# Performance work log

Measured on AMD Instinct MI355X. Metric: run time of the kernel, lower is better.

The kernel has to match this reference:

```python
import jax, jax.numpy as jnp
import numpy as np

# --- basis bookkeeping (mirrors TwoBodyToSpherical._generate_buffers) ---
METADATA = np.array([3, 2, 1], dtype=np.int64)          # shells per l
N_IRREPS = 2 * np.arange(3, dtype=np.int64) + 1          # 2l+1
REP_OFFSETS = np.concatenate([[0], np.cumsum(METADATA * N_IRREPS)[:-1]])
NUM_REPS_1D = int((METADATA * N_IRREPS).sum())           # = 14
M_IDX_MAP = {0: [0], 1: [0, 2, 1], 2: [0, 1, 2, 3, 4]}
ANGULAR = {"s": 0, "p": 1, "d": 2}

C_AOS = ["1s", "2s", "3s"] + ["2p"] * 3 + ["3p"] * 3 + ["3d"] * 5
H_AOS = ["1s", "2s"]


def _build_repid_map(aos):
    # faithful port of the per-element repid_map construction (valence_only=True)
    repid = np.zeros(len(aos), dtype=np.int64)
    dst_n, l_last, m_qc = 0, 0, 0
    for i, ao in enumerate(aos):
        l = ANGULAR[ao[1]]
        if l > l_last:
            dst_n = 0
        repid[i] = REP_OFFSETS[l] + dst_n + M_IDX_MAP[l][m_qc] * METADATA[l]
        if m_qc == 2 * l:
            m_qc = 0
            dst_n += 1
        else:
            m_qc += 1
        l_last = l
    return repid


def setup_inputs() -> dict:
    key = jax.random.key(0)
    maps = {"C": _build_repid_map(C_AOS), "H": _build_repid_map(H_AOS)}
    atomsybs = ["C"] * 400 + ["H"] * 100               # 500 atoms
    n_atoms = len(atomsybs)
    dst_rep_ids_1d = np.concatenate([maps[a] for a in atomsybs])
    lens = np.array([len(maps[a]) for a in atomsybs], dtype=np.int64)
    dst_offsets_1d = np.repeat(np.arange(n_atoms, dtype=np.int64), lens)
    dst_flat_ids_1d = dst_offsets_1d * NUM_REPS_1D + dst_rep_ids_1d  # [N_ao]=5800
    n_ao = dst_flat_ids_1d.shape[0]
    feat_ten = jax.random.normal(key, (n_ao, n_ao), dtype=jnp.float32)
    return {
        "feat_ten": feat_ten,
        "dst_flat_ids_1d": jnp.asarray(dst_flat_ids_1d, dtype=jnp.int32),
        "n_atoms": n_atoms,
        "num_reps_1d": NUM_REPS_1D,
    }


def reference(feat_ten, dst_flat_ids_1d, n_atoms, num_reps_1d):
    total = n_atoms * num_reps_1d                        # 7000
    # 2D destination flat ids: outer-sum of 1D ids (rep_dims=(0,1))
    ids2d = (dst_flat_ids_1d[:, None] * total + dst_flat_ids_1d[None, :]).reshape(-1)
    flat = feat_ten.reshape(-1)
    out_flat = jnp.zeros((total * total,), dtype=feat_ten.dtype).at[ids2d].add(flat)
    # view(n_atoms, R, n_atoms, R) then transpose(1,2) -> [A, A, R, R]
    out = out_flat.reshape(n_atoms, num_reps_1d, n_atoms, num_reps_1d)
    return jnp.transpose(out, (0, 2, 1, 3))
```

## Files before the change

kernel.cpp:

```cpp
#include <hip/hip_runtime.h>

constexpr int R = 14;
constexpr int A = 500;
constexpr int TOTAL = A * R;
constexpr int TILE = R * R;
constexpr int G = 25;
constexpr int NG = A / G;
constexpr int SUPER = 4;
constexpr int NSUP = NG / SUPER;
constexpr int MAXW = G * R;
constexpr int WP = 360;
constexpr int CHUNK = G * TILE;

__global__ __launch_bounds__(1024) void setup_kernel(
        const int* __restrict__ dst, int n_ao,
        int* __restrict__ inv, int* __restrict__ arow,
        int* __restrict__ ncols, int* __restrict__ pm) {
    int tid = threadIdx.x;
    for (int t = tid; t < TOTAL; t += 1024) inv[t] = -1;
    __syncthreads();
    for (int t = tid; t < n_ao; t += 1024) inv[dst[t]] = t;
    __syncthreads();
    if (tid < A) {
        int a = tid, lo = 0x7fffffff, hi = -1;
#pragma unroll
        for (int r = 0; r < R; ++r) {
            int v = inv[a * R + r];
            if (v >= 0) { lo = min(lo, v); hi = max(hi, v); }
        }
        arow[a] = lo;
        ncols[a] = hi - lo + 1;
#pragma unroll
        for (int r = 0; r < R; ++r) {
            int v = inv[a * R + r];
            pm[a * R + r] = (v >= 0) ? (v - lo) : -1;
        }
    }
}

__global__ __launch_bounds__(512) void tile_kernel(
        const float* __restrict__ feat,
        const int* __restrict__ arow,
        const int* __restrict__ ncols,
        const int* __restrict__ pm,
        float* __restrict__ out, int n_ao) {
    const int gs  = blockIdx.x % NSUP;
    const int a1  = blockIdx.x / NSUP;
    const int tid = threadIdx.x;

    __shared__ float buf[R][WP];
    __shared__ int s_pr[R];
    __shared__ int s_pc[G * R];
    __shared__ int s_off[G];

    const int arow1 = arow[a1];
    const int n1    = ncols[a1];
    if (tid < R) s_pr[tid] = pm[a1 * R + tid];

    const int d0 = tid >> 7;
    const int c4 = tid & 127;

    for (int s = 0; s < SUPER; ++s) {
        const int g0   = (gs * SUPER + s) * G;
        const int colL = arow[g0];
        const int colA = colL & ~3;
        const int colR = arow[g0 + G - 1] + ncols[g0 + G - 1];
        const int W4   = (colR - colA + 3) >> 2;

        for (int t = tid; t < G * R; t += 512) s_pc[t] = pm[g0 * R + t];
        if (tid < G) s_off[tid] = arow[g0 + tid] - colA;

        if (c4 < W4) {
            const float4* src4 =
                (const float4*)(feat + (long long)arow1 * n_ao + colA);
            const int rs4 = n_ao >> 2;
            for (int d = d0; d < n1; d += 4)
                *(float4*)&buf[d][c4 << 2] = src4[(long long)d * rs4 + c4];
        }
        __syncthreads();

        const long long outbase = ((long long)a1 * A + g0) * (long long)TILE;
        for (int o4 = tid * 4; o4 < CHUNK; o4 += 2048) {
            int a2i = o4 / TILE;
            int e   = o4 - a2i * TILE;
            int r1  = e / R;
            int r2  = e - r1 * R;
            int d   = s_pr[r1];
            int off = s_off[a2i];
            const int* pc = &s_pc[a2i * R];
            float4 v;
            float* vp = &v.x;
#pragma unroll
            for (int k = 0; k < 4; ++k) {
                int c = pc[r2];
                vp[k] = ((d | c) >= 0) ? buf[d][off + c] : 0.0f;
                if (++r2 == R) { r2 = 0; d = s_pr[++r1]; }
            }
            *reinterpret_cast<float4*>(out + outbase + o4) = v;
        }
        __syncthreads();
    }
}

extern "C" void kernel_launch(void* const* d_in, const int* in_sizes, int n_in,
                              void* d_out, int out_size, void* d_ws, size_t ws_size,
                              hipStream_t stream) {
    const float* feat = (const float*)d_in[0];
    const int*   dst  = (const int*)d_in[1];
    int n_ao = in_sizes[1];

    int* inv   = (int*)d_ws;
    int* arow  = inv + TOTAL;
    int* ncols = arow + A;
    int* pm    = ncols + A;

    setup_kernel<<<1, 1024, 0, stream>>>(dst, n_ao, inv, arow, ncols, pm);
    tile_kernel<<<A * NSUP, 512, 0, stream>>>(feat, arow, ncols, pm,
                                              (float*)d_out, n_ao);
}
```

Before: 317.1 us.

## Double-buffer staged feature rows and precompute per-thread gather indices

Double-buffers the shared-memory staging of source feature rows: the global loads for the next super-step are issued into registers before the current tile's gather and written to the other buffer afterwards, so one barrier per step is removed and load latency can overlap with output writes. All per-group column maps and offsets are loaded into shared memory once up front, and each thread's division/modulo index math is hoisted out of the loop. It also adds an occupancy hint to launch bounds. The cost is roughly double the shared memory and more registers per thread, which could limit occupancy.

```diff
diff --git a/kernel.cpp b/kernel.cpp
--- a/kernel.cpp
+++ b/kernel.cpp
@@ -8,8 +8,7 @@
 constexpr int NG = A / G;
 constexpr int SUPER = 4;
 constexpr int NSUP = NG / SUPER;
-constexpr int MAXW = G * R;
-constexpr int WP = 360;
+constexpr int WP = 356;
 constexpr int CHUNK = G * TILE;
 
 __global__ __launch_bounds__(1024) void setup_kernel(
@@ -38,7 +37,7 @@
     }
 }
 
-__global__ __launch_bounds__(512) void tile_kernel(
+__global__ __launch_bounds__(512, 6) void tile_kernel(
         const float* __restrict__ feat,
         const int* __restrict__ arow,
         const int* __restrict__ ncols,
@@ -48,57 +47,114 @@
     const int a1  = blockIdx.x / NSUP;
     const int tid = threadIdx.x;
 
-    __shared__ float buf[R][WP];
+    __shared__ float buf[2][R][WP];
     __shared__ int s_pr[R];
-    __shared__ int s_pc[G * R];
-    __shared__ int s_off[G];
+    __shared__ int s_pc[SUPER][G * R];
+    __shared__ int s_off[SUPER][G];
+    __shared__ int s_colA[SUPER];
+    __shared__ int s_W4[SUPER];
 
     const int arow1 = arow[a1];
     const int n1    = ncols[a1];
+    const int gbase = gs * (SUPER * G);
+
     if (tid < R) s_pr[tid] = pm[a1 * R + tid];
+    for (int t = tid; t < SUPER * G * R; t += 512)
+        (&s_pc[0][0])[t] = pm[gbase * R + t];
+    if (tid < SUPER) {
+        const int g0 = gbase + tid * G;
+        const int colA = arow[g0] & ~3;
+        s_colA[tid] = colA;
+        s_W4[tid]   = (arow[g0 + G - 1] + ncols[g0 + G - 1] - colA + 3) >> 2;
+    }
+    if (tid < SUPER * G) {
+        const int sI = tid / G, i = tid - sI * G;
+        const int g0 = gbase + sI * G;
+        s_off[sI][i] = arow[g0 + i] - (arow[g0] & ~3);
+    }
+    __syncthreads();
 
-    const int d0 = tid >> 7;
-    const int c4 = tid & 127;
+    int a2i_[3], dk_[3][4], ci_[3][4];
+    bool val_[3];
+#pragma unroll
+    for (int j = 0; j < 3; ++j) {
+        const int o4 = tid * 4 + j * 2048;
+        val_[j] = (o4 < CHUNK);
+        const int o = val_[j] ? o4 : 0;
+        int a2i = o / TILE;
+        int e   = o - a2i * TILE;
+        int r1  = e / R;
+        int r2  = e - r1 * R;
+        a2i_[j] = a2i;
+#pragma unroll
+        for (int k = 0; k < 4; ++k) {
+            dk_[j][k] = s_pr[r1];
+            ci_[j][k] = a2i * R + r2;
+            if (++r2 == R) { r2 = 0; ++r1; }
+        }
+    }
 
+    const int d0  = tid >> 7;
+    const int c4  = tid & 127;
+    const int rs4 = n_ao >> 2;
+    const float4* feat4 = reinterpret_cast<const float4*>(feat);
+
+    float4 rg[4];
+
+    auto stage_load = [&](int s) {
+        const int W4 = s_W4[s];
+        if (c4 < W4) {
+            const float4* src = feat4 + (long long)arow1 * rs4 + (s_colA[s] >> 2) + c4;
+#pragma unroll
+            for (int u = 0; u < 4; ++u) {
+                const int d = d0 + u * 4;
+                if (d < n1) rg[u] = src[(long long)d * rs4];
+            }
+        }
+    };
+    auto stage_write = [&](int nb, int s) {
+        const int W4 = s_W4[s];
+        if (c4 < W4) {
+#pragma unroll
+            for (int u = 0; u < 4; ++u) {
+                const int d = d0 + u * 4;
+                if (d < n1)
+                    *reinterpret_cast<float4*>(&buf[nb][d][c4 << 2]) = rg[u];
+            }
+        }
+    };
+
+    stage_load(0);
+    stage_write(0, 0);
+    __syncthreads();
+
+    int cb = 0;
     for (int s = 0; s < SUPER; ++s) {
-        const int g0   = (gs * SUPER + s) * G;
-        const int colL = arow[g0];
-        const int colA = colL & ~3;
-        const int colR = arow[g0 + G - 1] + ncols[g0 + G - 1];
-        const int W4   = (colR - colA + 3) >> 2;
+        if (s + 1 < SUPER) stage_load(s + 1);
 
-        for (int t = tid; t < G * R; t += 512) s_pc[t] = pm[g0 * R + t];
-        if (tid < G) s_off[tid] = arow[g0 + tid] - colA;
-
-        if (c4 < W4) {
-            const float4* src4 =
-                (const float4*)(feat + (long long)arow1 * n_ao + colA);
-            const int rs4 = n_ao >> 2;
-            for (int d = d0; d < n1; d += 4)
-                *(float4*)&buf[d][c4 << 2] = src4[(long long)d * rs4 + c4];
-        }
-        __syncthreads();
-
-        const long long outbase = ((long long)a1 * A + g0) * (long long)TILE;
-        for (int o4 = tid * 4; o4 < CHUNK; o4 += 2048) {
-            int a2i = o4 / TILE;
-            int e   = o4 - a2i * TILE;
-            int r1  = e / R;
-            int r2  = e - r1 * R;
-            int d   = s_pr[r1];
-            int off = s_off[a2i];
-            const int* pc = &s_pc[a2i * R];
+        const long long outbase =
+            ((long long)a1 * A + gbase + s * G) * (long long)TILE;
+        const int* pcS = &s_pc[s][0];
+#pragma unroll
+        for (int j = 0; j < 3; ++j) {
+            if (!val_[j]) continue;
+            const int off = s_off[s][a2i_[j]];
             float4 v;
             float* vp = &v.x;
 #pragma unroll
             for (int k = 0; k < 4; ++k) {
-                int c = pc[r2];
-                vp[k] = ((d | c) >= 0) ? buf[d][off + c] : 0.0f;
-                if (++r2 == R) { r2 = 0; d = s_pr[++r1]; }
+                const int d = dk_[j][k];
+                const int c = pcS[ci_[j][k]];
+                vp[k] = ((d | c) >= 0) ? buf[cb][d][off + c] : 0.0f;
             }
-            *reinterpret_cast<float4*>(out + outbase + o4) = v;
+            *reinterpret_cast<float4*>(out + outbase + tid * 4 + j * 2048) = v;
         }
-        __syncthreads();
+
+        if (s + 1 < SUPER) {
+            stage_write(cb ^ 1, s + 1);
+            __syncthreads();
+            cb ^= 1;
+        }
     }
 }
 
```

After: 351.5 us. +10.8%, slower.

## Replace LDS-staged tile copy with direct per-wave global gather

Applied to the files above, without the earlier changes.

Drops the shared-memory staging of feature row strips and instead has each wave gather each output tile's 196 elements straight from global memory, using precomputed row bases and column offsets. Each lane handles four consecutive tile elements across 25 destination atoms, and 256-thread blocks cover 100 atoms each. This removes the LDS round-trip and the per-superblock barriers. The cost is scattered, uncoalesced global reads that rely on cache hits, and 15 of every 64 lanes sit idle.

```diff
diff --git a/kernel.cpp b/kernel.cpp
--- a/kernel.cpp
+++ b/kernel.cpp
@@ -4,13 +4,10 @@
 constexpr int A = 500;
 constexpr int TOTAL = A * R;
 constexpr int TILE = R * R;
-constexpr int G = 25;
-constexpr int NG = A / G;
-constexpr int SUPER = 4;
-constexpr int NSUP = NG / SUPER;
-constexpr int MAXW = G * R;
-constexpr int WP = 360;
-constexpr int CHUNK = G * TILE;
+constexpr int APB = 100;
+constexpr int BPA = A / APB;
+constexpr int TPW = APB / 4;
+constexpr int SENT = (int)0xC0000000;
 
 __global__ __launch_bounds__(1024) void setup_kernel(
         const int* __restrict__ dst, int n_ao,
@@ -38,67 +35,54 @@
     }
 }
 
-__global__ __launch_bounds__(512) void tile_kernel(
+__global__ __launch_bounds__(256, 8) void gather_kernel(
         const float* __restrict__ feat,
         const int* __restrict__ arow,
-        const int* __restrict__ ncols,
         const int* __restrict__ pm,
         float* __restrict__ out, int n_ao) {
-    const int gs  = blockIdx.x % NSUP;
-    const int a1  = blockIdx.x / NSUP;
-    const int tid = threadIdx.x;
+    const int a1     = blockIdx.x / BPA;
+    const int a2base = (blockIdx.x % BPA) * APB;
+    const int tid    = threadIdx.x;
+    const int wave   = tid >> 6;
+    const int lane   = tid & 63;
 
-    __shared__ float buf[R][WP];
-    __shared__ int s_pr[R];
-    __shared__ int s_pc[G * R];
-    __shared__ int s_off[G];
+    __shared__ int s_cof[APB * R];
+    for (int t = tid; t < APB * R; t += 256) {
+        const int a2  = a2base + t / R;
+        const int pmv = pm[a2base * R + t];
+        s_cof[t] = (pmv >= 0) ? (arow[a2] + pmv) : SENT;
+    }
 
-    const int arow1 = arow[a1];
-    const int n1    = ncols[a1];
-    if (tid < R) s_pr[tid] = pm[a1 * R + tid];
+    const bool active = (lane < 49);
+    const int  e0     = active ? lane * 4 : 0;
+    const int  arow1  = arow[a1];
+    int rowb[4];
+    int r2o[4];
+#pragma unroll
+    for (int k = 0; k < 4; ++k) {
+        const int e  = e0 + k;
+        const int r1 = e / R;
+        r2o[k]       = e - r1 * R;
+        const int dd = pm[a1 * R + r1];
+        rowb[k] = (active && dd >= 0) ? (arow1 + dd) * n_ao : SENT;
+    }
+    __syncthreads();
 
-    const int d0 = tid >> 7;
-    const int c4 = tid & 127;
-
-    for (int s = 0; s < SUPER; ++s) {
-        const int g0   = (gs * SUPER + s) * G;
-        const int colL = arow[g0];
-        const int colA = colL & ~3;
-        const int colR = arow[g0 + G - 1] + ncols[g0 + G - 1];
-        const int W4   = (colR - colA + 3) >> 2;
-
-        for (int t = tid; t < G * R; t += 512) s_pc[t] = pm[g0 * R + t];
-        if (tid < G) s_off[tid] = arow[g0 + tid] - colA;
-
-        if (c4 < W4) {
-            const float4* src4 =
-                (const float4*)(feat + (long long)arow1 * n_ao + colA);
-            const int rs4 = n_ao >> 2;
-            for (int d = d0; d < n1; d += 4)
-                *(float4*)&buf[d][c4 << 2] = src4[(long long)d * rs4 + c4];
+    const int  i0 = wave * TPW;
+    float* const outw = out + ((long long)(a1 * A + a2base + i0)) * TILE
+                            + (lane << 2);
+#pragma unroll 2
+    for (int i = 0; i < TPW; ++i) {
+        const int* cof = &s_cof[(i0 + i) * R];
+        float4 v = make_float4(0.f, 0.f, 0.f, 0.f);
+        float* vp = &v.x;
+#pragma unroll
+        for (int k = 0; k < 4; ++k) {
+            const int ad = rowb[k] + cof[r2o[k]];
+            if (ad >= 0) vp[k] = feat[ad];
         }
-        __syncthreads();
-
-        const long long outbase = ((long long)a1 * A + g0) * (long long)TILE;
-        for (int o4 = tid * 4; o4 < CHUNK; o4 += 2048) {
-            int a2i = o4 / TILE;
-            int e   = o4 - a2i * TILE;
-            int r1  = e / R;
-            int r2  = e - r1 * R;
-            int d   = s_pr[r1];
-            int off = s_off[a2i];
-            const int* pc = &s_pc[a2i * R];
-            float4 v;
-            float* vp = &v.x;
-#pragma unroll
-            for (int k = 0; k < 4; ++k) {
-                int c = pc[r2];
-                vp[k] = ((d | c) >= 0) ? buf[d][off + c] : 0.0f;
-                if (++r2 == R) { r2 = 0; d = s_pr[++r1]; }
-            }
-            *reinterpret_cast<float4*>(out + outbase + o4) = v;
-        }
-        __syncthreads();
+        if (active)
+            *reinterpret_cast<float4*>(outw + (long long)i * TILE) = v;
     }
 }
 
@@ -115,6 +99,6 @@
     int* pm    = ncols + A;
 
     setup_kernel<<<1, 1024, 0, stream>>>(dst, n_ao, inv, arow, ncols, pm);
-    tile_kernel<<<A * NSUP, 512, 0, stream>>>(feat, arow, ncols, pm,
-                                              (float*)d_out, n_ao);
+    gather_kernel<<<A * BPA, 256, 0, stream>>>(feat, arow, pm,
+                                               (float*)d_out, n_ao);
 }
```

Result: slower. 378.1 us (+19.2%).
